# Performance work log

Hardware: AMD Instinct MI355X
Metric: run time of the kernel (lower is better)

Reference implementation:

```python
import jax, jax.numpy as jnp
import numpy as np


def setup_inputs() -> dict:
    key = jax.random.key(0)
    k1, k2, k3, k4 = jax.random.split(key, 4)
    B, T, E, H = 16, 2048, 1024, 128
    x = jax.random.normal(k1, (B, T, E), dtype=jnp.float32)
    Wk = jax.random.normal(k2, (E, H), dtype=jnp.float32) * (E ** -0.5)
    Wq = jax.random.normal(k3, (E, H), dtype=jnp.float32) * (E ** -0.5)
    Wv = jax.random.normal(k4, (E, H), dtype=jnp.float32) * (E ** -0.5)
    return {"x": x, "Wk": Wk, "Wq": Wq, "Wv": Wv}


def reference(x, Wk, Wq, Wv):
    # x: [B,T,E]; Wk/Wq/Wv: [E,H]
    B, T, E = x.shape
    H = Wk.shape[1]
    k = jnp.einsum('bte,eh->bth', x, Wk)
    q = jnp.einsum('bte,eh->bth', x, Wq)
    v = jnp.einsum('bte,eh->bth', x, Wv)
    # scores [B,T,T]; original masks with -inf THEN scales (equivalent math)
    scores = jnp.einsum('bqh,bkh->bqk', q, k) * (H ** -0.5)
    causal = jnp.tril(jnp.ones((T, T), dtype=bool))
    scores = jnp.where(causal, scores, -jnp.inf)
    weights = jax.nn.softmax(scores, axis=-1)
    # dropout disabled (eval mode reference)
    return jnp.einsum('bqk,bkh->bqh', weights, v)
```

## Files before the change

### kernel.cpp

```cpp
#include <hip/hip_runtime.h>

#define B_ 16
#define T_ 2048
#define E_ 1024
#define H_ 128

typedef short bf16x8 __attribute__((ext_vector_type(8)));
typedef float f32x4 __attribute__((ext_vector_type(4)));
typedef unsigned short u16x4 __attribute__((ext_vector_type(4)));

static __device__ __forceinline__ unsigned short f2bf(float f) {
    unsigned int u = __float_as_uint(f);
    u += 0x7FFFu + ((u >> 16) & 1u);
    return (unsigned short)(u >> 16);
}
static __device__ __forceinline__ unsigned int pk2(unsigned short a, unsigned short b) {
    return (unsigned int)a | ((unsigned int)b << 16);
}
static __device__ __forceinline__ bf16x8 frag(uint4 v) {
    return __builtin_bit_cast(bf16x8, v);
}
static __device__ __forceinline__ void gl16(const unsigned short* g, unsigned short* l) {
    __builtin_amdgcn_global_load_lds(
        (const __attribute__((address_space(1))) void*)g,
        (__attribute__((address_space(3))) void*)l, 16, 0, 0);
}

__global__ __launch_bounds__(256) void xcvt_kernel(
    const float* __restrict__ x, unsigned short* __restrict__ xb)
{
    size_t i = ((size_t)blockIdx.x * 256 + threadIdx.x) * 8;
    float4 a = *(const float4*)(x + i);
    float4 b = *(const float4*)(x + i + 4);
    uint4 o;
    o.x = pk2(f2bf(a.x), f2bf(a.y));
    o.y = pk2(f2bf(a.z), f2bf(a.w));
    o.z = pk2(f2bf(b.x), f2bf(b.y));
    o.w = pk2(f2bf(b.z), f2bf(b.w));
    *(uint4*)(xb + i) = o;
}

__global__ __launch_bounds__(256) void wcvt_kernel(
    const float* __restrict__ w0, const float* __restrict__ w1,
    const float* __restrict__ w2, unsigned short* __restrict__ wt)
{
    int g   = blockIdx.x * 256 + threadIdx.x;
    int arr = g >> 14;
    int rem = g & 16383;
    int h   = rem >> 7;
    int e0  = (rem & 127) * 8;
    const float* src = (arr == 0) ? w0 : (arr == 1) ? w1 : w2;
    unsigned short b[8];
#pragma unroll
    for (int i = 0; i < 8; i++) b[i] = f2bf(src[(size_t)(e0 + i) * H_ + h]);
    uint4 o;
    o.x = pk2(b[0], b[1]); o.y = pk2(b[2], b[3]);
    o.z = pk2(b[4], b[5]); o.w = pk2(b[6], b[7]);
    *(uint4*)&wt[(size_t)(arr * 128 + h) * E_ + e0] = o;
}

__global__ __launch_bounds__(256, 3) void proj_kernel(
    const unsigned short* __restrict__ xb,
    const unsigned short* __restrict__ wt,
    unsigned short* __restrict__ q_ws,
    unsigned short* __restrict__ kp_ws,
    unsigned short* __restrict__ vt_ws)
{
    const int m0 = blockIdx.x * 128;
    const int by = blockIdx.y;
    __shared__ __align__(16) unsigned short As[128 * 32];
    __shared__ __align__(16) unsigned short Bs[128 * 32];

    const int tid  = threadIdx.x;
    const int lane = tid & 63;
    const int w    = tid >> 6;
    const int quad = lane >> 4;
    const int lm   = lane & 15;
    const int rw   = (w & 1) * 64;
    const int cw   = (w >> 1) * 64;

    const int srow = w * 32 + (lane >> 2);
    const int sch  = (lane & 3) * 8;
    const unsigned short* ga0 = xb + (size_t)(m0 + srow) * E_ + sch;
    const unsigned short* ga1 = ga0 + (size_t)16 * E_;
    const unsigned short* gb0 = wt + (size_t)(by * 128 + srow) * E_ + sch;
    const unsigned short* gb1 = gb0 + (size_t)16 * E_;
    unsigned short* la0 = As + (size_t)(w * 2)     * 512;
    unsigned short* la1 = As + (size_t)(w * 2 + 1) * 512;
    unsigned short* lb0 = Bs + (size_t)(w * 2)     * 512;
    unsigned short* lb1 = Bs + (size_t)(w * 2 + 1) * 512;

    const f32x4 z4 = {0.f, 0.f, 0.f, 0.f};
    f32x4 acc[4][4];
#pragma unroll
    for (int i = 0; i < 4; i++)
#pragma unroll
        for (int j = 0; j < 4; j++) acc[i][j] = z4;

    for (int kb = 0; kb < 32; kb++) {
        __syncthreads();
        gl16(ga0, la0); gl16(ga1, la1);
        gl16(gb0, lb0); gl16(gb1, lb1);
        __syncthreads();
        ga0 += 32; ga1 += 32; gb0 += 32; gb1 += 32;

        bf16x8 a[4], b[4];
#pragma unroll
        for (int am = 0; am < 4; am++)
            a[am] = frag(*(const uint4*)&As[(rw + am * 16 + lm) * 32 + quad * 8]);
#pragma unroll
        for (int bn = 0; bn < 4; bn++)
            b[bn] = frag(*(const uint4*)&Bs[(cw + bn * 16 + lm) * 32 + quad * 8]);
#pragma unroll
        for (int am = 0; am < 4; am++)
#pragma unroll
            for (int bn = 0; bn < 4; bn++)
                acc[am][bn] = __builtin_amdgcn_mfma_f32_16x16x32_bf16(
                    a[am], b[bn], acc[am][bn], 0, 0, 0);
    }

    const int bb = m0 >> 11;
    const int t0 = m0 & 2047;
#pragma unroll
    for (int am = 0; am < 4; am++)
#pragma unroll
        for (int bn = 0; bn < 4; bn++) {
            const int col = cw + bn * 16 + lm;
            if (by == 0) {
                const int row = m0 + rw + am * 16 + quad * 4;
#pragma unroll
                for (int r = 0; r < 4; r++)
                    q_ws[(size_t)(row + r) * H_ + col] = f2bf(acc[am][bn][r]);
            } else if (by == 1) {
                const int tl = t0 + rw + am * 16 + quad * 4;
#pragma unroll
                for (int r = 0; r < 4; r++) {
                    int t = tl + r;
                    kp_ws[(size_t)(bb * 64 + (t >> 5)) * 4096 +
                          (col >> 5) * 1024 + (t & 31) * 32 + (col & 31)] =
                        f2bf(acc[am][bn][r]);
                }
            } else {
                const int tt = t0 + rw + am * 16 + quad * 4;
                u16x4 p;
#pragma unroll
                for (int r = 0; r < 4; r++) p[r] = f2bf(acc[am][bn][r]);
                *(u16x4*)&vt_ws[((size_t)(bb * 64 + (tt >> 5)) * 128 + col) * 32 + (tt & 31)] = p;
            }
        }
}

__global__ __launch_bounds__(256, 4) void attn_kernel(
    const unsigned short* __restrict__ q_ws,
    const unsigned short* __restrict__ kp_ws,
    const unsigned short* __restrict__ vt_ws,
    float* __restrict__ out,
    int* __restrict__ ctr)
{
    __shared__ __align__(16) unsigned short Ks[4096];
    __shared__ __align__(16) unsigned short Vs[4096];
    __shared__ __align__(16) unsigned short Ps[4][16][40];
    __shared__ int s_task;

    const int tid  = threadIdx.x;
    const int lane = tid & 63;
    const int ww   = tid >> 6;
    const int quad = lane >> 4;
    const int lm   = lane & 15;
    const float scale = 0.08838834764831845f;

    bf16x8 ones;
#pragma unroll
    for (int i = 0; i < 8; i++) ones[i] = (short)0x3F80;
    const f32x4 z4 = {0.f, 0.f, 0.f, 0.f};

    const int so = ww * 1024 + lane * 8;
    unsigned short* lk0 = Ks + ww * 1024;
    unsigned short* lk1 = Ks + ww * 1024 + 512;
    unsigned short* lv0 = Vs + ww * 1024;
    unsigned short* lv1 = Vs + ww * 1024 + 512;

    for (;;) {
        __syncthreads();
        if (tid == 0) s_task = atomicAdd(ctr, 1);
        __syncthreads();
        const int s = s_task;
        if (s >= 512) break;
        const int tau   = 31 - (s >> 4);
        const int batch = s & 15;
        const size_t bq = (size_t)batch * T_ * H_;
        const unsigned short* Kt = kp_ws + (size_t)(batch * 64) * 4096 + so;
        const unsigned short* Vt = vt_ws + (size_t)(batch * 64) * 4096 + so;

        bf16x8 qf[4];
#pragma unroll
        for (int h = 0; h < 4; h++)
            qf[h] = frag(*(const uint4*)(q_ws + bq +
                     (size_t)(tau * 64 + ww * 16 + lm) * H_ + h * 32 + quad * 8));

        f32x4 o[9];
#pragma unroll
        for (int f = 0; f < 9; f++) o[f] = z4;

        const int nkt = 2 * tau + 2;
        for (int kt = 0; kt < nkt; kt++) {
            __syncthreads();
            const unsigned short* kg = Kt + (size_t)kt * 4096;
            const unsigned short* vg = Vt + (size_t)kt * 4096;
            gl16(kg, lk0); gl16(kg + 512, lk1);
            gl16(vg, lv0); gl16(vg + 512, lv1);
            __syncthreads();

            f32x4 st0 = z4, st1 = z4;
#pragma unroll
            for (int h = 0; h < 4; h++) {
                bf16x8 kf0 = frag(*(const uint4*)&Ks[(h * 32 + lm) * 32 + quad * 8]);
                bf16x8 kf1 = frag(*(const uint4*)&Ks[(h * 32 + 16 + lm) * 32 + quad * 8]);
                st0 = __builtin_amdgcn_mfma_f32_16x16x32_bf16(kf0, qf[h], st0, 0, 0, 0);
                st1 = __builtin_amdgcn_mfma_f32_16x16x32_bf16(kf1, qf[h], st1, 0, 0, 0);
            }

            const int qg = tau * 64 + ww * 16 + lm;
            const int k0 = kt * 32;
            u16x4 pa, pb;
#pragma unroll
            for (int r = 0; r < 4; r++) {
                int kv0 = k0 + quad * 4 + r;
                float e0 = __expf(st0[r] * scale);
                float e1 = __expf(st1[r] * scale);
                pa[r] = (kv0      <= qg) ? f2bf(e0) : (unsigned short)0;
                pb[r] = (kv0 + 16 <= qg) ? f2bf(e1) : (unsigned short)0;
            }
            *(u16x4*)&Ps[ww][lm][quad * 4]      = pa;
            *(u16x4*)&Ps[ww][lm][16 + quad * 4] = pb;
            bf16x8 pf = frag(*(const uint4*)&Ps[ww][lm][quad * 8]);

#pragma unroll
            for (int f = 0; f < 8; f++) {
                bf16x8 vfr = frag(*(const uint4*)&Vs[(f * 16 + lm) * 32 + quad * 8]);
                o[f] = __builtin_amdgcn_mfma_f32_16x16x32_bf16(pf, vfr, o[f], 0, 0, 0);
            }
            o[8] = __builtin_amdgcn_mfma_f32_16x16x32_bf16(pf, ones, o[8], 0, 0, 0);
        }

        float* op = out + bq + (size_t)(tau * 64 + ww * 16) * H_;
#pragma unroll
        for (int r = 0; r < 4; r++) {
            float inv = 1.f / o[8][r];
#pragma unroll
            for (int f = 0; f < 8; f++)
                op[(size_t)(quad * 4 + r) * H_ + f * 16 + lm] = o[f][r] * inv;
        }
    }
}

extern "C" void kernel_launch(void* const* d_in, const int* in_sizes, int n_in,
                              void* d_out, int out_size, void* d_ws, size_t ws_size,
                              hipStream_t stream)
{
    const float* x  = (const float*)d_in[0];
    const float* Wk = (const float*)d_in[1];
    const float* Wq = (const float*)d_in[2];
    const float* Wv = (const float*)d_in[3];
    float* out = (float*)d_out;

    const size_t MH = (size_t)B_ * T_ * H_;
    const size_t ME = (size_t)B_ * T_ * E_;
    unsigned short* q_ws  = (unsigned short*)d_ws;
    unsigned short* kp_ws = q_ws + MH;
    unsigned short* vt_ws = kp_ws + MH;
    unsigned short* wt    = vt_ws + MH;
    unsigned short* xb    = wt + (size_t)384 * E_;
    int* ctr = (int*)(xb + ME);

    hipMemsetAsync(ctr, 0, 4, stream);
    xcvt_kernel<<<dim3(ME / 2048), dim3(256), 0, stream>>>(x, xb);
    wcvt_kernel<<<dim3(192), dim3(256), 0, stream>>>(Wq, Wk, Wv, wt);
    proj_kernel<<<dim3(256, 3), dim3(256), 0, stream>>>(xb, wt, q_ws, kp_ws, vt_ws);
    attn_kernel<<<dim3(256), dim3(256), 0, stream>>>(q_ws, kp_ws, vt_ws, out, ctr);
}
```

Before: 306.3 us.

## Double-buffer K/V tiles, statically pair causal tiles, and merge conversion kernels

The attention kernel now double-buffers the K and V LDS tiles, prefetching the next key tile while the current one is being computed, which removes one barrier per iteration and hides global load latency. The atomic work-queue scheduler is replaced with a static one in which each block handles query tile p and tile 31-p, giving every block the same amount of work; this also drops the counter memset. The x and weight fp32-to-bf16 conversion kernels are merged into one launch. In exchange, LDS use doubles and the launch bound drops to 2 blocks per CU, and the static split gives up dynamic load balancing.

```diff
diff --git a/kernel.cpp b/kernel.cpp
--- a/kernel.cpp
+++ b/kernel.cpp
@@ -26,37 +26,37 @@
         (__attribute__((address_space(3))) void*)l, 16, 0, 0);
 }
 
-__global__ __launch_bounds__(256) void xcvt_kernel(
-    const float* __restrict__ x, unsigned short* __restrict__ xb)
-{
-    size_t i = ((size_t)blockIdx.x * 256 + threadIdx.x) * 8;
-    float4 a = *(const float4*)(x + i);
-    float4 b = *(const float4*)(x + i + 4);
-    uint4 o;
-    o.x = pk2(f2bf(a.x), f2bf(a.y));
-    o.y = pk2(f2bf(a.z), f2bf(a.w));
-    o.z = pk2(f2bf(b.x), f2bf(b.y));
-    o.w = pk2(f2bf(b.z), f2bf(b.w));
-    *(uint4*)(xb + i) = o;
-}
-
-__global__ __launch_bounds__(256) void wcvt_kernel(
+__global__ __launch_bounds__(256) void cvt_kernel(
+    const float* __restrict__ x,
     const float* __restrict__ w0, const float* __restrict__ w1,
-    const float* __restrict__ w2, unsigned short* __restrict__ wt)
-{
-    int g   = blockIdx.x * 256 + threadIdx.x;
-    int arr = g >> 14;
-    int rem = g & 16383;
-    int h   = rem >> 7;
-    int e0  = (rem & 127) * 8;
-    const float* src = (arr == 0) ? w0 : (arr == 1) ? w1 : w2;
-    unsigned short b[8];
-#pragma unroll
-    for (int i = 0; i < 8; i++) b[i] = f2bf(src[(size_t)(e0 + i) * H_ + h]);
-    uint4 o;
-    o.x = pk2(b[0], b[1]); o.y = pk2(b[2], b[3]);
-    o.z = pk2(b[4], b[5]); o.w = pk2(b[6], b[7]);
-    *(uint4*)&wt[(size_t)(arr * 128 + h) * E_ + e0] = o;
+    const float* __restrict__ w2,
+    unsigned short* __restrict__ xb, unsigned short* __restrict__ wt)
+{
+    if (blockIdx.x < 16384) {
+        size_t i = ((size_t)blockIdx.x * 256 + threadIdx.x) * 8;
+        float4 a = *(const float4*)(x + i);
+        float4 b = *(const float4*)(x + i + 4);
+        uint4 o;
+        o.x = pk2(f2bf(a.x), f2bf(a.y));
+        o.y = pk2(f2bf(a.z), f2bf(a.w));
+        o.z = pk2(f2bf(b.x), f2bf(b.y));
+        o.w = pk2(f2bf(b.z), f2bf(b.w));
+        *(uint4*)(xb + i) = o;
+    } else {
+        int g   = (blockIdx.x - 16384) * 256 + threadIdx.x;
+        int arr = g >> 14;
+        int rem = g & 16383;
+        int h   = rem >> 7;
+        int e0  = (rem & 127) * 8;
+        const float* src = (arr == 0) ? w0 : (arr == 1) ? w1 : w2;
+        unsigned short b[8];
+#pragma unroll
+        for (int i = 0; i < 8; i++) b[i] = f2bf(src[(size_t)(e0 + i) * H_ + h]);
+        uint4 o;
+        o.x = pk2(b[0], b[1]); o.y = pk2(b[2], b[3]);
+        o.z = pk2(b[4], b[5]); o.w = pk2(b[6], b[7]);
+        *(uint4*)&wt[(size_t)(arr * 128 + h) * E_ + e0] = o;
+    }
 }
 
 __global__ __launch_bounds__(256, 3) void proj_kernel(
@@ -150,17 +150,18 @@
         }
 }
 
-__global__ __launch_bounds__(256, 4) void attn_kernel(
+__global__ __launch_bounds__(256, 2) void attn_kernel(
     const unsigned short* __restrict__ q_ws,
     const unsigned short* __restrict__ kp_ws,
     const unsigned short* __restrict__ vt_ws,
-    float* __restrict__ out,
-    int* __restrict__ ctr)
-{
-    __shared__ __align__(16) unsigned short Ks[4096];
-    __shared__ __align__(16) unsigned short Vs[4096];
+    float* __restrict__ out)
+{
+    __shared__ __align__(16) unsigned short Ks[2][4096];
+    __shared__ __align__(16) unsigned short Vs[2][4096];
     __shared__ __align__(16) unsigned short Ps[4][16][40];
-    __shared__ int s_task;
+
+    const int batch = blockIdx.x & 15;
+    const int p     = blockIdx.x >> 4;
 
     const int tid  = threadIdx.x;
     const int lane = tid & 63;
@@ -174,23 +175,15 @@
     for (int i = 0; i < 8; i++) ones[i] = (short)0x3F80;
     const f32x4 z4 = {0.f, 0.f, 0.f, 0.f};
 
+    const size_t bq = (size_t)batch * T_ * H_;
     const int so = ww * 1024 + lane * 8;
-    unsigned short* lk0 = Ks + ww * 1024;
-    unsigned short* lk1 = Ks + ww * 1024 + 512;
-    unsigned short* lv0 = Vs + ww * 1024;
-    unsigned short* lv1 = Vs + ww * 1024 + 512;
-
-    for (;;) {
-        __syncthreads();
-        if (tid == 0) s_task = atomicAdd(ctr, 1);
-        __syncthreads();
-        const int s = s_task;
-        if (s >= 512) break;
-        const int tau   = 31 - (s >> 4);
-        const int batch = s & 15;
-        const size_t bq = (size_t)batch * T_ * H_;
-        const unsigned short* Kt = kp_ws + (size_t)(batch * 64) * 4096 + so;
-        const unsigned short* Vt = vt_ws + (size_t)(batch * 64) * 4096 + so;
+    const unsigned short* Kt = kp_ws + (size_t)(batch * 64) * 4096 + so;
+    const unsigned short* Vt = vt_ws + (size_t)(batch * 64) * 4096 + so;
+
+#pragma unroll 1
+    for (int pi = 0; pi < 2; pi++) {
+        const int tau = pi ? (31 - p) : p;
+        const int nkt = 2 * tau + 2;
 
         bf16x8 qf[4];
 #pragma unroll
@@ -202,20 +195,26 @@
 #pragma unroll
         for (int f = 0; f < 9; f++) o[f] = z4;
 
-        const int nkt = 2 * tau + 2;
+        gl16(Kt, &Ks[0][ww * 1024]); gl16(Kt + 512, &Ks[0][ww * 1024 + 512]);
+        gl16(Vt, &Vs[0][ww * 1024]); gl16(Vt + 512, &Vs[0][ww * 1024 + 512]);
+
         for (int kt = 0; kt < nkt; kt++) {
+            const int cb = kt & 1;
             __syncthreads();
-            const unsigned short* kg = Kt + (size_t)kt * 4096;
-            const unsigned short* vg = Vt + (size_t)kt * 4096;
-            gl16(kg, lk0); gl16(kg + 512, lk1);
-            gl16(vg, lv0); gl16(vg + 512, lv1);
-            __syncthreads();
+
+            if (kt + 1 < nkt) {
+                const int nb = cb ^ 1;
+                const unsigned short* kg = Kt + (size_t)(kt + 1) * 4096;
+                const unsigned short* vg = Vt + (size_t)(kt + 1) * 4096;
+                gl16(kg, &Ks[nb][ww * 1024]); gl16(kg + 512, &Ks[nb][ww * 1024 + 512]);
+                gl16(vg, &Vs[nb][ww * 1024]); gl16(vg + 512, &Vs[nb][ww * 1024 + 512]);
+            }
 
             f32x4 st0 = z4, st1 = z4;
 #pragma unroll
             for (int h = 0; h < 4; h++) {
-                bf16x8 kf0 = frag(*(const uint4*)&Ks[(h * 32 + lm) * 32 + quad * 8]);
-                bf16x8 kf1 = frag(*(const uint4*)&Ks[(h * 32 + 16 + lm) * 32 + quad * 8]);
+                bf16x8 kf0 = frag(*(const uint4*)&Ks[cb][(h * 32 + lm) * 32 + quad * 8]);
+                bf16x8 kf1 = frag(*(const uint4*)&Ks[cb][(h * 32 + 16 + lm) * 32 + quad * 8]);
                 st0 = __builtin_amdgcn_mfma_f32_16x16x32_bf16(kf0, qf[h], st0, 0, 0, 0);
                 st1 = __builtin_amdgcn_mfma_f32_16x16x32_bf16(kf1, qf[h], st1, 0, 0, 0);
             }
@@ -237,7 +236,7 @@
 
 #pragma unroll
             for (int f = 0; f < 8; f++) {
-                bf16x8 vfr = frag(*(const uint4*)&Vs[(f * 16 + lm) * 32 + quad * 8]);
+                bf16x8 vfr = frag(*(const uint4*)&Vs[cb][(f * 16 + lm) * 32 + quad * 8]);
                 o[f] = __builtin_amdgcn_mfma_f32_16x16x32_bf16(pf, vfr, o[f], 0, 0, 0);
             }
             o[8] = __builtin_amdgcn_mfma_f32_16x16x32_bf16(pf, ones, o[8], 0, 0, 0);
@@ -251,6 +250,7 @@
             for (int f = 0; f < 8; f++)
                 op[(size_t)(quad * 4 + r) * H_ + f * 16 + lm] = o[f][r] * inv;
         }
+        __syncthreads();
     }
 }
 
@@ -271,11 +271,8 @@
     unsigned short* vt_ws = kp_ws + MH;
     unsigned short* wt    = vt_ws + MH;
     unsigned short* xb    = wt + (size_t)384 * E_;
-    int* ctr = (int*)(xb + ME);
-
-    hipMemsetAsync(ctr, 0, 4, stream);
-    xcvt_kernel<<<dim3(ME / 2048), dim3(256), 0, stream>>>(x, xb);
-    wcvt_kernel<<<dim3(192), dim3(256), 0, stream>>>(Wq, Wk, Wv, wt);
+
+    cvt_kernel<<<dim3(16576), dim3(256), 0, stream>>>(x, Wq, Wk, Wv, xb, wt);
     proj_kernel<<<dim3(256, 3), dim3(256), 0, stream>>>(xb, wt, q_ws, kp_ws, vt_ws);
-    attn_kernel<<<dim3(256), dim3(256), 0, stream>>>(q_ws, kp_ws, vt_ws, out, ctr);
-}
+    attn_kernel<<<dim3(256), dim3(256), 0, stream>>>(q_ws, kp_ws, vt_ws, out);
+}
```

Result: faster. 299.3 us (-2.3%).
